# Optimization experiments

Measured on AMD Instinct MI355X. Metric: run time of the kernel, lower is better.

Reference implementation:

```python
import jax, jax.numpy as jnp
import numpy as np

B, H, W, C = 8, 112, 112, 192
NH = 6
HD = C // NH
WS = 7            # window size
SS = 3            # shift size (WS//2)
N = WS * WS       # tokens per window (49)
NW = (H // WS) * (W // WS)  # windows per image
EPS = 1e-5
LOG100 = float(np.log(100.0))


def _rel_bias_consts():
    # continuous relative coords table, shape ((2*WS-1)^2, 2), log-spaced
    r = np.arange(-(WS - 1), WS, dtype=np.float32)
    table = np.stack(np.meshgrid(r, r, indexing='ij')).transpose(1, 2, 0).reshape(-1, 2)
    table = table / float(max(WS - 1, 1)) * 8.0
    table = np.sign(table) * np.log2(np.abs(table) + 1.0) / np.log2(8.0)
    # relative position index, shape (N*N,)
    coords = np.stack(np.meshgrid(np.arange(WS), np.arange(WS), indexing='ij')).reshape(2, -1)
    rel = (coords[:, :, None] - coords[:, None, :]).transpose(1, 2, 0) + (WS - 1)
    idx = (rel * np.array([2 * WS - 1, 1])).sum(-1).astype(np.int32).reshape(-1)
    return jnp.asarray(table), jnp.asarray(idx)


def _shift_attn_mask():
    # standard Swin shifted-window attention mask, shape (NW, N, N)
    img = np.zeros((H, W), np.float32)
    cnt = 0
    for hs in (slice(0, -WS), slice(-WS, -SS), slice(-SS, None)):
        for ws_ in (slice(0, -WS), slice(-WS, -SS), slice(-SS, None)):
            img[hs, ws_] = cnt
            cnt += 1
    win = img.reshape(H // WS, WS, W // WS, WS).transpose(0, 2, 1, 3).reshape(-1, N)
    diff = win[:, None, :] - win[:, :, None]
    return jnp.asarray(np.where(diff != 0, -100.0, 0.0).astype(np.float32))


_TABLE, _IDX = _rel_bias_consts()
_MASK = _shift_attn_mask()


def _ln(x, g, b):
    m = jnp.mean(x, axis=-1, keepdims=True)
    v = jnp.mean((x - m) ** 2, axis=-1, keepdims=True)
    return (x - m) / jnp.sqrt(v + EPS) * g + b


def setup_inputs() -> dict:
    key = jax.random.key(0)
    ks = jax.random.split(key, 8)
    s = 0.02
    return {
        'x': jax.random.normal(ks[0], (B, H * W, C), jnp.float32),
        'ln1_g': jnp.ones((C,), jnp.float32), 'ln1_b': jnp.zeros((C,), jnp.float32),
        'ln2_g': jnp.ones((C,), jnp.float32), 'ln2_b': jnp.zeros((C,), jnp.float32),
        'q_w': jax.random.normal(ks[1], (C, C), jnp.float32) * s,
        'q_b': jnp.zeros((C,), jnp.float32),
        'k_w': jax.random.normal(ks[2], (C, C), jnp.float32) * s,
        'v_w': jax.random.normal(ks[3], (C, C), jnp.float32) * s,
        'v_b': jnp.zeros((C,), jnp.float32),
        'p_w': jax.random.normal(ks[4], (C, C), jnp.float32) * s,
        'p_b': jnp.zeros((C,), jnp.float32),
        'logit_scale': jnp.log(10.0 * jnp.ones((NH, 1, 1), jnp.float32)),
        'cpb_w0': jax.random.normal(ks[5], (2, 512), jnp.float32) * s,
        'cpb_b0': jnp.zeros((512,), jnp.float32),
        'cpb_w1': jax.random.normal(ks[6], (512, NH), jnp.float32) * s,
        'fc1_w': jax.random.normal(ks[7], (C, 4 * C), jnp.float32) * s,
        'fc1_b': jnp.zeros((4 * C,), jnp.float32),
        'fc2_w': jax.random.normal(jax.random.fold_in(key, 9), (4 * C, C), jnp.float32) * s,
        'fc2_b': jnp.zeros((C,), jnp.float32),
    }


def reference(x, ln1_g, ln1_b, ln2_g, ln2_b, q_w, q_b, k_w, v_w, v_b, p_w, p_b,
              logit_scale, cpb_w0, cpb_b0, cpb_w1, fc1_w, fc1_b, fc2_w, fc2_b):
    shortcut = x
    h = x.reshape(B, H, W, C)
    h = jnp.roll(h, (-SS, -SS), axis=(1, 2))                       # cyclic shift
    # window partition -> (B*NW, N, C)
    win = h.reshape(B, H // WS, WS, W // WS, WS, C).transpose(0, 1, 3, 2, 4, 5)
    win = win.reshape(B * NW, N, C)

    q = (win @ q_w + q_b).reshape(-1, N, NH, HD).transpose(0, 2, 1, 3)  # (BW,h,N,d)
    k = (win @ k_w).reshape(-1, N, NH, HD).transpose(0, 2, 1, 3)
    v = (win @ v_w + v_b).reshape(-1, N, NH, HD).transpose(0, 2, 1, 3)

    # cosine attention with learned clamped logit scale
    qn = q / jnp.maximum(jnp.linalg.norm(q, axis=-1, keepdims=True), 1e-12)
    kn = k / jnp.maximum(jnp.linalg.norm(k, axis=-1, keepdims=True), 1e-12)
    scale = jnp.exp(jnp.minimum(logit_scale, LOG100))              # (h,1,1)
    attn = jnp.einsum('whqd,whkd->whqk', qn, kn) * scale

    # continuous relative position bias: MLP(2->512->h), gather, 16*sigmoid
    t = jax.nn.relu(_TABLE @ cpb_w0 + cpb_b0) @ cpb_w1             # ((2WS-1)^2, h)
    bias = t[_IDX].reshape(N, N, NH).transpose(2, 0, 1)            # (h,N,N)
    attn = attn + 16.0 * jax.nn.sigmoid(bias)[None]

    # shifted-window mask
    attn = attn.reshape(B, NW, NH, N, N) + _MASK[None, :, None]
    attn = jax.nn.softmax(attn.reshape(B * NW, NH, N, N), axis=-1)

    out = jnp.einsum('whqk,whkd->whqd', attn, v)                   # (BW,h,N,d)
    out = out.transpose(0, 2, 1, 3).reshape(B * NW, N, C)
    out = out @ p_w + p_b

    # window reverse + un-shift
    out = out.reshape(B, H // WS, W // WS, WS, WS, C).transpose(0, 1, 3, 2, 4, 5)
    out = out.reshape(B, H, W, C)
    out = jnp.roll(out, (SS, SS), axis=(1, 2)).reshape(B, H * W, C)

    # swin-v2 res-post-norm residuals
    hidden = shortcut + _ln(out, ln1_g, ln1_b)
    mlp = jax.nn.gelu(hidden @ fc1_w + fc1_b) @ fc2_w + fc2_b
    return hidden + _ln(mlp, ln2_g, ln2_b)
```

## Files before the change

### kernel.cpp

```cpp
#include <hip/hip_runtime.h>


typedef __bf16  bf16x8 __attribute__((ext_vector_type(8)));
typedef float   f32x4  __attribute__((ext_vector_type(4)));

__device__ __forceinline__ float bf2f(unsigned short u){
    return __uint_as_float(((unsigned int)u) << 16);
}
__device__ __forceinline__ unsigned short f2bf(float f){
    unsigned int u = __float_as_uint(f);
    unsigned int r = (u + 0x7fffu + ((u >> 16) & 1u)) >> 16;
    return (unsigned short)r;
}
__device__ __forceinline__ float ldin(const void* p, size_t i, int f32){
    return f32 ? ((const float*)p)[i] : bf2f(((const unsigned short*)p)[i]);
}
__device__ __forceinline__ void gl_lds16(const unsigned short* g, unsigned short* l){
    __builtin_amdgcn_global_load_lds(
        (const __attribute__((address_space(1))) unsigned int*)g,
        (__attribute__((address_space(3))) unsigned int*)l, 16, 0, 0);
}

__global__ void detect_kernel(const unsigned short* __restrict__ ln1g, int* __restrict__ flag){
    if (threadIdx.x == 0) *flag = (ln1g[0] == 0x3F80u) ? 0 : 1;
}

__global__ __launch_bounds__(256)
void pack_kernel(const void* __restrict__ qw, const void* __restrict__ kw,
                 const void* __restrict__ vw, const void* __restrict__ qb,
                 const void* __restrict__ vb, const void* __restrict__ pw,
                 const void* __restrict__ pb, const void* __restrict__ f1w,
                 const void* __restrict__ f1b, const void* __restrict__ f2w,
                 const void* __restrict__ f2b,
                 const void* __restrict__ l1g, const void* __restrict__ l1b,
                 const void* __restrict__ l2g, const void* __restrict__ l2b,
                 unsigned short* __restrict__ wqkvt, unsigned short* __restrict__ pwt,
                 unsigned short* __restrict__ f1t, unsigned short* __restrict__ f2t,
                 float* __restrict__ qkv_bias, float* __restrict__ p_bias,
                 float* __restrict__ f1_bias, float* __restrict__ f2_bias,
                 float* __restrict__ lnp, const int* __restrict__ dtf)
{
    int f32 = *dtf;
    int i = blockIdx.x * 256 + threadIdx.x;
    if (i < 110592){
        int n = i / 192, k = i - n * 192;
        float s = (n < 192) ? ldin(qw, (size_t)k*192 + n, f32)
                 : (n < 384) ? ldin(kw, (size_t)k*192 + (n-192), f32)
                 : ldin(vw, (size_t)k*192 + (n-384), f32);
        wqkvt[n*192 + k] = f2bf(s);
    }
    if (i < 36864){
        int n = i / 192, k = i - n * 192;
        pwt[n*192 + k] = f2bf(ldin(pw, (size_t)k*192 + n, f32));
    }
    if (i < 147456){
        int n = i / 192, k = i - n * 192;
        f1t[n*192 + k] = f2bf(ldin(f1w, (size_t)k*768 + n, f32));
        int n2 = i / 768, k2 = i - n2 * 768;
        f2t[n2*768 + k2] = f2bf(ldin(f2w, (size_t)k2*192 + n2, f32));
    }
    if (i < 576) qkv_bias[i] = (i < 192) ? ldin(qb, i, f32)
                              : (i < 384) ? 0.f : ldin(vb, i-384, f32);
    if (i < 192){
        p_bias[i]  = ldin(pb, i, f32);
        f2_bias[i] = ldin(f2b, i, f32);
        lnp[i]       = ldin(l1g, i, f32);
        lnp[192+i]   = ldin(l1b, i, f32);
        lnp[384+i]   = ldin(l2g, i, f32);
        lnp[576+i]   = ldin(l2b, i, f32);
    }
    if (i < 768) f1_bias[i] = ldin(f1b, i, f32);
}

__device__ __forceinline__ float cpb_coord(int a){
    float v = (float)(a - 6) * (8.0f / 6.0f);
    float s = (v > 0.f) ? 1.f : (v < 0.f ? -1.f : 0.f);
    return s * log2f(fabsf(v) + 1.f) * (1.f / 3.f);
}

__global__ __launch_bounds__(256)
void cpb_kernel(const void* __restrict__ ls, const void* __restrict__ w0,
                const void* __restrict__ b0, const void* __restrict__ w1,
                float* __restrict__ bmask, float* __restrict__ scale,
                const int* __restrict__ dtf)
{
    __shared__ float w0a[512], w0b[512], b0s[512], w1s[512];
    __shared__ float tv[169];
    __shared__ float sval[2401];
    int f32 = *dtf;
    int tid = threadIdx.x;
    int h = blockIdx.x;

    for (int c = tid; c < 512; c += 256){
        w0a[c] = ldin(w0, c, f32);
        w0b[c] = ldin(w0, 512 + c, f32);
        b0s[c] = ldin(b0, c, f32);
        w1s[c] = ldin(w1, (size_t)c*6 + h, f32);
    }
    __syncthreads();

    for (int q = tid; q < 169; q += 256){
        int a = q / 13, b = q - a * 13;
        float t0 = cpb_coord(a), t1 = cpb_coord(b);
        float acc = 0.f;
        for (int c = 0; c < 512; ++c){
            float hv = fmaxf(t0 * w0a[c] + t1 * w0b[c] + b0s[c], 0.f);
            acc += hv * w1s[c];
        }
        tv[q] = acc;
    }
    __syncthreads();

    for (int e = tid; e < 2401; e += 256){
        int i = e / 49, j = e - i * 49;
        int di = i/7 - j/7 + 6;
        int dj = (i - (i/7)*7) - (j - (j/7)*7) + 6;
        sval[e] = 16.f / (1.f + expf(-tv[di*13 + dj]));
    }
    __syncthreads();

    for (int t = 0; t < 4; ++t){
        int ey = t >> 1, ex = t & 1;
        for (int e = tid; e < 4096; e += 256){
            int row = e >> 6, li = e & 63;
            int lrow = li >> 2, f = li & 3;
            int col = f*16 + lrow;
            float val;
            if (row >= 49) val = 0.f;
            else if (col >= 49) val = -1e30f;
            else {
                val = sval[row*49 + col];
                int rr = row/7, rc = row - rr*7;
                int cr = col/7, cc = col - cr*7;
                int ridr = (ey ? (rr < 4 ? 1 : 2) : 0)*3 + (ex ? (rc < 4 ? 1 : 2) : 0);
                int ridc = (ey ? (cr < 4 ? 1 : 2) : 0)*3 + (ex ? (cc < 4 ? 1 : 2) : 0);
                if (ridr != ridc) val -= 100.f;
            }
            bmask[(((size_t)(h*4 + t)*64 + row) << 6) + li] = val;
        }
    }
    if (tid == 0) scale[h] = expf(fminf(ldin(ls, h, f32), 4.6051702f));
}

template<int GATHER, int EPI>
__device__ __forceinline__ size_t gemm_aoff(int t, int K){
    if (GATHER){
        int w = t / 49, p = t - w * 49;
        int bb = w >> 8, widx = w & 255;
        int wy = widx >> 4, wx = widx & 15;
        int r = p / 7, c = p - r * 7;
        int oy = (wy*7 + r + 3) % 112;
        int ox = (wx*7 + c + 3) % 112;
        return ((size_t)bb * 12544 + (size_t)oy * 112 + ox) * 192;
    }
    return (size_t)t * K;
}

template<int GATHER, int EPI>
__global__ __launch_bounds__(256)
void gemm_kernel(const void* __restrict__ A,
                 const unsigned short* __restrict__ Bt,
                 const float* __restrict__ bias,
                 unsigned short* __restrict__ Cout,
                 int M, int N, int K, const int* __restrict__ dtf)
{
    __shared__ unsigned short As[128][32];
    __shared__ unsigned short Bs[192][32];

    int f32 = GATHER ? *dtf : 0;
    int tid = threadIdx.x;
    int nb = N / 192;
    int bng = blockIdx.x % nb;
    int bm  = (blockIdx.x / nb) * 128;
    int bn0 = bng * 192;

    int wv = tid >> 6, ln = tid & 63;
    int lrow4 = ln >> 2, lseg = ln & 3;

    const unsigned short* Ag0; const unsigned short* Ag1;
    {
        int r0 = bm + wv*32 + lrow4;
        Ag0 = (const unsigned short*)A + gemm_aoff<GATHER,EPI>(r0, K) + lseg*8;
        Ag1 = (const unsigned short*)A + gemm_aoff<GATHER,EPI>(r0 + 16, K) + lseg*8;
    }
    const unsigned short* Bg = Bt + (size_t)(bn0 + wv*48 + lrow4) * K + lseg*8;
    size_t bstep = (size_t)16 * K;

    int arow = tid >> 2, aseg = tid & 3;
    size_t aoff0 = 0, aoff1 = 0;
    const unsigned short *brp0 = 0, *brp1 = 0, *brp2 = 0;
    if (GATHER && f32){
        aoff0 = gemm_aoff<GATHER,EPI>(bm + arow, K);
        aoff1 = gemm_aoff<GATHER,EPI>(bm + arow + 64, K);
        brp0 = Bt + (size_t)(bn0       + arow) * K;
        brp1 = Bt + (size_t)(bn0 +  64 + arow) * K;
        brp2 = Bt + (size_t)(bn0 + 128 + arow) * K;
    }

    int wm = wv * 32;
    int quad = ln >> 4, lrow = ln & 15;

    f32x4 acc[12][2] = {};

    for (int k0 = 0; k0 < K; k0 += 32){
        __syncthreads();
        if (GATHER && f32){
            const float* p0 = (const float*)A + aoff0 + k0 + aseg*8;
            const float* p1 = (const float*)A + aoff1 + k0 + aseg*8;
            unsigned short t8[8];
            #pragma unroll
            for (int j = 0; j < 8; ++j) t8[j] = f2bf(p0[j]);
            *(uint4*)(&As[arow][aseg*8]) = *(const uint4*)t8;
            #pragma unroll
            for (int j = 0; j < 8; ++j) t8[j] = f2bf(p1[j]);
            *(uint4*)(&As[arow + 64][aseg*8]) = *(const uint4*)t8;
            *(uint4*)(&Bs[arow      ][aseg*8]) = *(const uint4*)(brp0 + k0 + aseg*8);
            *(uint4*)(&Bs[arow +  64][aseg*8]) = *(const uint4*)(brp1 + k0 + aseg*8);
            *(uint4*)(&Bs[arow + 128][aseg*8]) = *(const uint4*)(brp2 + k0 + aseg*8);
        } else {
            gl_lds16(Ag0 + k0, &As[wv*32     ][0]);
            gl_lds16(Ag1 + k0, &As[wv*32 + 16][0]);
            gl_lds16(Bg  + k0,             &Bs[wv*48     ][0]);
            gl_lds16(Bg  + bstep + k0,     &Bs[wv*48 + 16][0]);
            gl_lds16(Bg  + 2*bstep + k0,   &Bs[wv*48 + 32][0]);
        }
        __syncthreads();
        bf16x8 a0 = *(const bf16x8*)(&As[wm      + lrow][quad*8]);
        bf16x8 a1 = *(const bf16x8*)(&As[wm + 16 + lrow][quad*8]);
        #pragma unroll
        for (int f = 0; f < 12; ++f){
            bf16x8 bb = *(const bf16x8*)(&Bs[f*16 + lrow][quad*8]);
            acc[f][0] = __builtin_amdgcn_mfma_f32_16x16x32_bf16(a0, bb, acc[f][0], 0, 0, 0);
            acc[f][1] = __builtin_amdgcn_mfma_f32_16x16x32_bf16(a1, bb, acc[f][1], 0, 0, 0);
        }
    }

    #pragma unroll
    for (int f = 0; f < 12; ++f)
    #pragma unroll
    for (int tm = 0; tm < 2; ++tm)
    #pragma unroll
    for (int i = 0; i < 4; ++i){
        int row = bm + wm + tm*16 + quad*4 + i;
        int col = bn0 + f*16 + lrow;
        float v = acc[f][tm][i] + bias[col];
        if (EPI == 1){
            float t = __expf(v * fmaf(v*v, -0.071354816f, -1.5957691216f));
            v = v * __builtin_amdgcn_rcpf(1.f + t);
        }
        Cout[(size_t)row * N + col] = f2bf(v);
    }
}

__global__ __launch_bounds__(256)
void attn_kernel(const unsigned short* __restrict__ qkv,
                 const float* __restrict__ bmask,
                 const float* __restrict__ scale,
                 unsigned short* __restrict__ attn_out)
{
    __shared__ unsigned short qb[64][40];
    __shared__ unsigned short kb[64][40];
    __shared__ unsigned short vT[32][72];
    __shared__ unsigned short Ps[64][72];
    __shared__ float rnq[64], rnk[64];

    int tid = threadIdx.x;
    int w = blockIdx.x, h = blockIdx.y;
    int widx = w & 255;
    int wy = widx >> 4, wx = widx & 15;
    int mtype = ((wy == 15) ? 2 : 0) | ((wx == 15) ? 1 : 0);

    size_t wbase = (size_t)w * 49 * 576 + (size_t)h * 32;

    for (int e = tid; e < 512; e += 256){
        int p = e >> 3, s = e & 7;
        uint2 zq = {0u, 0u}, zk = {0u, 0u};
        if (p < 49){
            size_t g = wbase + (size_t)p * 576 + s * 4;
            zq = *(const uint2*)&qkv[g];
            zk = *(const uint2*)&qkv[g + 192];
        }
        *(uint2*)&qb[p][s*4] = zq;
        *(uint2*)&kb[p][s*4] = zk;
    }
    for (int e = tid; e < 2048; e += 256){
        int p = e >> 5, d = e & 31;
        vT[d][p] = (p < 49) ? qkv[wbase + (size_t)p * 576 + 384 + d]
                            : (unsigned short)0;
    }
    __syncthreads();

    {
        int row = tid >> 2, seg = tid & 3;
        bf16x8 qv = *(const bf16x8*)&qb[row][seg * 8];
        bf16x8 kv = *(const bf16x8*)&kb[row][seg * 8];
        float q2 = 0.f, k2 = 0.f;
        #pragma unroll
        for (int j = 0; j < 8; ++j){
            float a = (float)qv[j], b = (float)kv[j];
            q2 = fmaf(a, a, q2);
            k2 = fmaf(b, b, k2);
        }
        q2 += __shfl_xor(q2, 1);  q2 += __shfl_xor(q2, 2);
        k2 += __shfl_xor(k2, 1);  k2 += __shfl_xor(k2, 2);
        if (seg == 0){
            rnq[row] = scale[h] * rsqrtf(fmaxf(q2, 1e-24f));
            rnk[row] = rsqrtf(fmaxf(k2, 1e-24f));
        }
    }
    __syncthreads();

    int wave = tid >> 6, lane = tid & 63;
    int quad = lane >> 4, lrow = lane & 15;
    int wm = wave * 16;

    bf16x8 aq = *(const bf16x8*)&qb[wm + lrow][quad * 8];
    f32x4 sfr[4];
    #pragma unroll
    for (int f = 0; f < 4; ++f){
        bf16x8 bk = *(const bf16x8*)&kb[f*16 + lrow][quad * 8];
        f32x4 z = {0.f, 0.f, 0.f, 0.f};
        sfr[f] = __builtin_amdgcn_mfma_f32_16x16x32_bf16(aq, bk, z, 0, 0, 0);
    }

    float rk[4];
    #pragma unroll
    for (int f = 0; f < 4; ++f) rk[f] = rnk[f*16 + lrow];
    const float4* bmp = (const float4*)bmask + (size_t)(h*4 + mtype) * 1024;
    #pragma unroll
    for (int reg = 0; reg < 4; ++reg){
        int row = wm + quad*4 + reg;
        float rq = rnq[row];
        float4 bm = bmp[row*16 + lrow];
        float v0 = fmaf(sfr[0][reg], rq*rk[0], bm.x);
        float v1 = fmaf(sfr[1][reg], rq*rk[1], bm.y);
        float v2 = fmaf(sfr[2][reg], rq*rk[2], bm.z);
        float v3 = fmaf(sfr[3][reg], rq*rk[3], bm.w);
        float mx = fmaxf(fmaxf(v0, v1), fmaxf(v2, v3));
        #pragma unroll
        for (int m = 8; m; m >>= 1) mx = fmaxf(mx, __shfl_xor(mx, m));
        float e0 = __expf(v0 - mx), e1 = __expf(v1 - mx);
        float e2 = __expf(v2 - mx), e3 = __expf(v3 - mx);
        float sm = (e0 + e1) + (e2 + e3);
        #pragma unroll
        for (int m = 8; m; m >>= 1) sm += __shfl_xor(sm, m);
        float inv = 1.f / sm;
        Ps[row][ 0 + lrow] = f2bf(e0 * inv);
        Ps[row][16 + lrow] = f2bf(e1 * inv);
        Ps[row][32 + lrow] = f2bf(e2 * inv);
        Ps[row][48 + lrow] = f2bf(e3 * inv);
    }
    __syncthreads();

    f32x4 o[2] = {{0.f,0.f,0.f,0.f}, {0.f,0.f,0.f,0.f}};
    #pragma unroll
    for (int c = 0; c < 2; ++c){
        bf16x8 ap = *(const bf16x8*)&Ps[wm + lrow][c*32 + quad*8];
        #pragma unroll
        for (int n = 0; n < 2; ++n){
            bf16x8 bv = *(const bf16x8*)&vT[n*16 + lrow][c*32 + quad*8];
            o[n] = __builtin_amdgcn_mfma_f32_16x16x32_bf16(ap, bv, o[n], 0, 0, 0);
        }
    }
    __syncthreads();

    unsigned short (*Os)[40] = qb;
    #pragma unroll
    for (int n = 0; n < 2; ++n)
    #pragma unroll
    for (int reg = 0; reg < 4; ++reg){
        int row = wm + quad*4 + reg;
        if (row < 49) Os[row][n*16 + lrow] = f2bf(o[n][reg]);
    }
    __syncthreads();

    for (int e = tid; e < 392; e += 256){
        int p = e >> 3, c4 = (e & 7) * 4;
        uint2 val = *(const uint2*)&Os[p][c4];
        *(uint2*)&attn_out[((size_t)w*49 + p)*192 + (size_t)h*32 + c4] = val;
    }
}

template<int FINAL>
__global__ __launch_bounds__(256)
void ln_kernel(const void* __restrict__ base,
               const unsigned short* __restrict__ src,
               const float* __restrict__ g,
               const float* __restrict__ b,
               void* __restrict__ dst, const int* __restrict__ dtf)
{
    int f32 = *dtf;
    int tid = threadIdx.x;
    int lane = tid & 63;
    int token = blockIdx.x * 4 + (tid >> 6);

    size_t srow;
    if (FINAL){
        srow = (size_t)token * 192;
    } else {
        int bb = token / 12544, pix = token - bb*12544;
        int y = pix / 112, x = pix - y*112;
        int gy = (y + 109) % 112, gx = (x + 109) % 112;
        int wy = gy / 7, r = gy - wy*7;
        int wx = gx / 7, c = gx - wx*7;
        int t = (bb*256 + wy*16 + wx)*49 + r*7 + c;
        srow = (size_t)t * 192;
    }

    float o[3]; float s = 0.f;
    #pragma unroll
    for (int j = 0; j < 3; ++j){ o[j] = bf2f(src[srow + j*64 + lane]); s += o[j]; }
    #pragma unroll
    for (int off = 32; off; off >>= 1) s += __shfl_xor(s, off);
    float m = s * (1.f/192.f);
    float vsum = 0.f;
    #pragma unroll
    for (int j = 0; j < 3; ++j){ float d = o[j] - m; vsum += d*d; }
    #pragma unroll
    for (int off = 32; off; off >>= 1) vsum += __shfl_xor(vsum, off);
    float rstd = rsqrtf(vsum * (1.f/192.f) + 1e-5f);

    size_t brow = (size_t)token * 192;
    #pragma unroll
    for (int j = 0; j < 3; ++j){
        int cidx = j*64 + lane;
        float bv = FINAL ? bf2f(((const unsigned short*)base)[brow + cidx])
                         : ldin(base, brow + cidx, f32);
        float val = bv + (o[j] - m) * rstd * g[cidx] + b[cidx];
        if (FINAL){
            if (f32) ((float*)dst)[brow + cidx] = val;
            else     ((unsigned short*)dst)[brow + cidx] = f2bf(val);
        } else {
            ((unsigned short*)dst)[brow + cidx] = f2bf(val);
        }
    }
}

extern "C" void kernel_launch(void* const* d_in, const int* in_sizes, int n_in,
                              void* d_out, int out_size, void* d_ws, size_t ws_size,
                              hipStream_t stream)
{
    const void* x    = d_in[0];
    const void* ln1g = d_in[1];
    const void* ln1b = d_in[2];
    const void* ln2g = d_in[3];
    const void* ln2b = d_in[4];
    const void* qw   = d_in[5];
    const void* qb   = d_in[6];
    const void* kw   = d_in[7];
    const void* vw   = d_in[8];
    const void* vb   = d_in[9];
    const void* pw   = d_in[10];
    const void* pb   = d_in[11];
    const void* ls   = d_in[12];
    const void* w0   = d_in[13];
    const void* b0   = d_in[14];
    const void* w1   = d_in[15];
    const void* f1w  = d_in[16];
    const void* f1b  = d_in[17];
    const void* f2w  = d_in[18];
    const void* f2b  = d_in[19];

    char* ws = (char*)d_ws;
    unsigned short* big    = (unsigned short*)(ws);
    unsigned short* bufB   = (unsigned short*)(ws + 154140672);
    unsigned short* hidden = (unsigned short*)(ws + 192675840);
    unsigned short* wqkvt  = (unsigned short*)(ws + 231211008);
    unsigned short* pwt    = (unsigned short*)(ws + 231211008 + 221184);
    unsigned short* f1t    = (unsigned short*)(ws + 231211008 + 221184 + 73728);
    unsigned short* f2t    = (unsigned short*)(ws + 231211008 + 221184 + 73728 + 294912);
    float* qkv_bias = (float*)(ws + 232095744);
    float* p_bias   = qkv_bias + 576;
    float* f1_bias  = p_bias + 192;
    float* f2_bias  = f1_bias + 768;
    float* bmask    = (float*)(ws + 232102656);
    float* scale    = (float*)(ws + 232495872);
    float* lnp      = (float*)(ws + 232495896);
    int*   dtf      = (int*)  (ws + 232498968);

    detect_kernel<<<1, 64, 0, stream>>>((const unsigned short*)ln1g, dtf);
    pack_kernel<<<576, 256, 0, stream>>>(qw, kw, vw, qb, vb, pw, pb, f1w, f1b, f2w, f2b,
                                         ln1g, ln1b, ln2g, ln2b,
                                         wqkvt, pwt, f1t, f2t,
                                         qkv_bias, p_bias, f1_bias, f2_bias, lnp, dtf);
    cpb_kernel<<<6, 256, 0, stream>>>(ls, w0, b0, w1, bmask, scale, dtf);

    gemm_kernel<1,0><<<784*3, 256, 0, stream>>>(x, wqkvt, qkv_bias, big, 100352, 576, 192, dtf);
    attn_kernel<<<dim3(2048, 6), 256, 0, stream>>>(big, bmask, scale, bufB);
    gemm_kernel<0,0><<<784, 256, 0, stream>>>(bufB, pwt, p_bias, big, 100352, 192, 192, dtf);
    ln_kernel<0><<<25088, 256, 0, stream>>>(x, big, lnp, lnp + 192, hidden, dtf);
    gemm_kernel<0,1><<<784*4, 256, 0, stream>>>(hidden, f1t, f1_bias, big, 100352, 768, 192, dtf);
    gemm_kernel<0,0><<<784, 256, 0, stream>>>(big, f2t, f2_bias, bufB, 100352, 192, 768, dtf);
    ln_kernel<1><<<25088, 256, 0, stream>>>(hidden, bufB, lnp + 384, lnp + 576, d_out, dtf);

    (void)in_sizes; (void)n_in; (void)out_size; (void)ws_size;
}
```

Before: 555.2 us.

## Double-buffer LDS tiles in GEMM to overlap global loads with MFMA

```diff
diff --git a/kernel.cpp b/kernel.cpp
--- a/kernel.cpp
+++ b/kernel.cpp
@@ -164,8 +164,8 @@
                  unsigned short* __restrict__ Cout,
                  int M, int N, int K, const int* __restrict__ dtf)
 {
-    __shared__ unsigned short As[128][32];
-    __shared__ unsigned short Bs[192][32];
+    __shared__ unsigned short As[2][128][32];
+    __shared__ unsigned short Bs[2][192][32];
 
     int f32 = GATHER ? *dtf : 0;
     int tid = threadIdx.x;
@@ -186,52 +186,70 @@
     const unsigned short* Bg = Bt + (size_t)(bn0 + wv*48 + lrow4) * K + lseg*8;
     size_t bstep = (size_t)16 * K;
 
-    int arow = tid >> 2, aseg = tid & 3;
-    size_t aoff0 = 0, aoff1 = 0;
-    const unsigned short *brp0 = 0, *brp1 = 0, *brp2 = 0;
-    if (GATHER && f32){
-        aoff0 = gemm_aoff<GATHER,EPI>(bm + arow, K);
-        aoff1 = gemm_aoff<GATHER,EPI>(bm + arow + 64, K);
-        brp0 = Bt + (size_t)(bn0       + arow) * K;
-        brp1 = Bt + (size_t)(bn0 +  64 + arow) * K;
-        brp2 = Bt + (size_t)(bn0 + 128 + arow) * K;
-    }
-
     int wm = wv * 32;
     int quad = ln >> 4, lrow = ln & 15;
 
     f32x4 acc[12][2] = {};
 
-    for (int k0 = 0; k0 < K; k0 += 32){
-        __syncthreads();
-        if (GATHER && f32){
+    if (GATHER && f32){
+        int arow = tid >> 2, aseg = tid & 3;
+        size_t aoff0 = gemm_aoff<GATHER,EPI>(bm + arow, K);
+        size_t aoff1 = gemm_aoff<GATHER,EPI>(bm + arow + 64, K);
+        const unsigned short* brp0 = Bt + (size_t)(bn0       + arow) * K;
+        const unsigned short* brp1 = Bt + (size_t)(bn0 +  64 + arow) * K;
+        const unsigned short* brp2 = Bt + (size_t)(bn0 + 128 + arow) * K;
+        for (int k0 = 0; k0 < K; k0 += 32){
+            __syncthreads();
             const float* p0 = (const float*)A + aoff0 + k0 + aseg*8;
             const float* p1 = (const float*)A + aoff1 + k0 + aseg*8;
             unsigned short t8[8];
             #pragma unroll
             for (int j = 0; j < 8; ++j) t8[j] = f2bf(p0[j]);
-            *(uint4*)(&As[arow][aseg*8]) = *(const uint4*)t8;
+            *(uint4*)(&As[0][arow][aseg*8]) = *(const uint4*)t8;
             #pragma unroll
             for (int j = 0; j < 8; ++j) t8[j] = f2bf(p1[j]);
-            *(uint4*)(&As[arow + 64][aseg*8]) = *(const uint4*)t8;
-            *(uint4*)(&Bs[arow      ][aseg*8]) = *(const uint4*)(brp0 + k0 + aseg*8);
-            *(uint4*)(&Bs[arow +  64][aseg*8]) = *(const uint4*)(brp1 + k0 + aseg*8);
-            *(uint4*)(&Bs[arow + 128][aseg*8]) = *(const uint4*)(brp2 + k0 + aseg*8);
-        } else {
-            gl_lds16(Ag0 + k0, &As[wv*32     ][0]);
-            gl_lds16(Ag1 + k0, &As[wv*32 + 16][0]);
-            gl_lds16(Bg  + k0,             &Bs[wv*48     ][0]);
-            gl_lds16(Bg  + bstep + k0,     &Bs[wv*48 + 16][0]);
-            gl_lds16(Bg  + 2*bstep + k0,   &Bs[wv*48 + 32][0]);
-        }
-        __syncthreads();
-        bf16x8 a0 = *(const bf16x8*)(&As[wm      + lrow][quad*8]);
-        bf16x8 a1 = *(const bf16x8*)(&As[wm + 16 + lrow][quad*8]);
-        #pragma unroll
-        for (int f = 0; f < 12; ++f){
-            bf16x8 bb = *(const bf16x8*)(&Bs[f*16 + lrow][quad*8]);
-            acc[f][0] = __builtin_amdgcn_mfma_f32_16x16x32_bf16(a0, bb, acc[f][0], 0, 0, 0);
-            acc[f][1] = __builtin_amdgcn_mfma_f32_16x16x32_bf16(a1, bb, acc[f][1], 0, 0, 0);
+            *(uint4*)(&As[0][arow + 64][aseg*8]) = *(const uint4*)t8;
+            *(uint4*)(&Bs[0][arow      ][aseg*8]) = *(const uint4*)(brp0 + k0 + aseg*8);
+            *(uint4*)(&Bs[0][arow +  64][aseg*8]) = *(const uint4*)(brp1 + k0 + aseg*8);
+            *(uint4*)(&Bs[0][arow + 128][aseg*8]) = *(const uint4*)(brp2 + k0 + aseg*8);
+            __syncthreads();
+            bf16x8 a0 = *(const bf16x8*)(&As[0][wm      + lrow][quad*8]);
+            bf16x8 a1 = *(const bf16x8*)(&As[0][wm + 16 + lrow][quad*8]);
+            #pragma unroll
+            for (int f = 0; f < 12; ++f){
+                bf16x8 bb = *(const bf16x8*)(&Bs[0][f*16 + lrow][quad*8]);
+                acc[f][0] = __builtin_amdgcn_mfma_f32_16x16x32_bf16(a0, bb, acc[f][0], 0, 0, 0);
+                acc[f][1] = __builtin_amdgcn_mfma_f32_16x16x32_bf16(a1, bb, acc[f][1], 0, 0, 0);
+            }
+        }
+    } else {
+        gl_lds16(Ag0,                 &As[0][wv*32     ][0]);
+        gl_lds16(Ag1,                 &As[0][wv*32 + 16][0]);
+        gl_lds16(Bg,                  &Bs[0][wv*48     ][0]);
+        gl_lds16(Bg + bstep,          &Bs[0][wv*48 + 16][0]);
+        gl_lds16(Bg + 2*bstep,        &Bs[0][wv*48 + 32][0]);
+        int cur = 0;
+        for (int k0 = 0; k0 < K; k0 += 32){
+            asm volatile("s_waitcnt vmcnt(0)" ::: "memory");
+            __builtin_amdgcn_s_barrier();
+            __builtin_amdgcn_sched_barrier(0);
+            if (k0 + 32 < K){
+                int nk = k0 + 32, nb_ = cur ^ 1;
+                gl_lds16(Ag0 + nk,            &As[nb_][wv*32     ][0]);
+                gl_lds16(Ag1 + nk,            &As[nb_][wv*32 + 16][0]);
+                gl_lds16(Bg  + nk,            &Bs[nb_][wv*48     ][0]);
+                gl_lds16(Bg  + bstep + nk,    &Bs[nb_][wv*48 + 16][0]);
+                gl_lds16(Bg  + 2*bstep + nk,  &Bs[nb_][wv*48 + 32][0]);
+            }
+            bf16x8 a0 = *(const bf16x8*)(&As[cur][wm      + lrow][quad*8]);
+            bf16x8 a1 = *(const bf16x8*)(&As[cur][wm + 16 + lrow][quad*8]);
+            #pragma unroll
+            for (int f = 0; f < 12; ++f){
+                bf16x8 bb = *(const bf16x8*)(&Bs[cur][f*16 + lrow][quad*8]);
+                acc[f][0] = __builtin_amdgcn_mfma_f32_16x16x32_bf16(a0, bb, acc[f][0], 0, 0, 0);
+                acc[f][1] = __builtin_amdgcn_mfma_f32_16x16x32_bf16(a1, bb, acc[f][1], 0, 0, 0);
+            }
+            cur ^= 1;
         }
     }
 
```

Result: faster. 535.7 us (-3.5%).
